# Kernel tuning notes

Measured on AMD Instinct MI355X. Metric: run time of the kernel, lower is better.

## Reference

```python
import jax, jax.numpy as jnp
import numpy as np

SR = 44100
S_TAUS = [10.0, 50.0, 100.0]   # ms
L_TAUS = [500.0, 1500.0, 3000.0]  # ms
EPS = 1e-8


def ms2coef(ms, sr):
    return float(1.0 - np.exp(-2200.0 / (ms * sr)))


def ema(x, coef):
    # First-order leaky integrator y[t] = coef*x[t] + (1-coef)*y[t-1], y[-1]=0.
    # x: [B, T]; scan over time with carry of shape [B].
    coef = jnp.asarray(coef, x.dtype)
    one_m = jnp.asarray(1.0, x.dtype) - coef

    def step(carry, xt):
        y = coef * xt + one_m * carry
        return y, y

    _, ys = jax.lax.scan(step, jnp.zeros(x.shape[0], x.dtype), x.T)
    return ys.T  # [B, T]


def hadamard(x):
    # mid/side transform on channel dim (-2), orthonormal scaling
    m = x[..., 0, :] + x[..., 1, :]
    s = x[..., 0, :] - x[..., 1, :]
    return jnp.stack([m, s], axis=-2) * jnp.asarray(np.sqrt(0.5), x.dtype)


def ldr_feat(x_sq, s_coef, l_coef, shift):
    # log short-term envelope minus (time-aligned) log long-term envelope
    short = jnp.log(ema(x_sq, s_coef))
    long_ = jnp.log(ema(x_sq, l_coef))
    return short - jnp.roll(long_, -shift, axis=-1)


def setup_inputs() -> dict:
    key = jax.random.key(0)
    k1, k2 = jax.random.split(key)
    x_pred = jax.random.normal(k1, (4, 2, 1048576), dtype=jnp.float32)
    x_true = jax.random.normal(k2, (4, 2, 1048576), dtype=jnp.float32)
    return {"x_pred": x_pred, "x_true": x_true}


def reference(x_pred, x_true):
    xp = hadamard(x_pred)
    xt = hadamard(x_true)
    T = xp.shape[-1]
    ps = jnp.clip(jnp.square(xp), EPS, None).reshape(-1, T)
    ts = jnp.clip(jnp.square(xt), EPS, None).reshape(-1, T)
    total = jnp.asarray(0.0, x_pred.dtype)
    for s_ms, l_ms in zip(S_TAUS, L_TAUS):
        sc = ms2coef(s_ms, SR)
        lc = ms2coef(l_ms, SR)
        shift = int(SR * (l_ms - s_ms) * 0.0005)
        fp = ldr_feat(ps, sc, lc, shift)
        ft = ldr_feat(ts, sc, lc, shift)
        total = total + jnp.mean(jnp.abs(fp - ft))
    return total
```

## Files before the change

kernel.cpp:

```cpp
#include <hip/hip_runtime.h>
#include <cmath>


#define T_LEN    1048576
#define CHUNKS   256
#define CLEN     4096
#define NT1      256
#define SEG1     16
#define COLS     65536
#define JMAX     65535
#define EPS_CLIP 1e-8f
#define K2SEG    32
#define K2NSEG   8

struct K1Args {
  float d[6];
  float apw[6][7];
};
struct K2Args {
  float dL[6];
  float dL32[6];
};
struct CarryPack {
  float d[3];
  float apw[3][9];
};

__device__ __constant__ const int D_SHIFT[3] = {10804, 31972, 63945};


__global__ __launch_bounds__(NT1)
void k1_stage(const float* __restrict__ xp, const float* __restrict__ xt,
              float* __restrict__ Eloc, float* __restrict__ Bs,
              float* __restrict__ Bl, int mode, K1Args ka)
{
  int chunk = blockIdx.x, b = blockIdx.y;
  int which = b >> 2, sig = b & 3, tid = threadIdx.x;
  long base = (long)chunk * CLEN + (long)tid * SEG1;
  const float* x0 = (which ? xt : xp) + (long)sig * 2 * T_LEN;
  const float* x1 = x0 + T_LEN;

  float S[12];
#pragma unroll
  for (int j = 0; j < 12; j++) S[j] = 0.f;

#pragma unroll
  for (int i = 0; i < SEG1 / 4; i++) {
    float4 a = *(const float4*)(x0 + base + 4*i);
    float4 c4 = *(const float4*)(x1 + base + 4*i);
    float sm, sp, pm, ps;
#define STEP(CMP) \
    sm = a.CMP + c4.CMP; sp = a.CMP - c4.CMP; \
    pm = fmaxf(0.5f * sm * sm, EPS_CLIP); ps = fmaxf(0.5f * sp * sp, EPS_CLIP); \
    _Pragma("unroll") \
    for (int cf = 0; cf < 6; cf++) { \
      S[cf*2+0] = fmaf(ka.d[cf], S[cf*2+0], pm); \
      S[cf*2+1] = fmaf(ka.d[cf], S[cf*2+1], ps); \
    }
    STEP(x) STEP(y) STEP(z) STEP(w)
#undef STEP
  }

  int lane = tid & 63, w = tid >> 6;
#pragma unroll
  for (int i = 0; i < 6; i++) {
#pragma unroll
    for (int j = 0; j < 12; j++) {
      float up = __shfl_up(S[j], 1u << i, 64);
      if (lane >= (1 << i)) S[j] = fmaf(ka.apw[j >> 1][i], up, S[j]);
    }
  }
  __shared__ float WT[4][12];
  if (lane == 63)
#pragma unroll
    for (int j = 0; j < 12; j++) WT[w][j] = S[j];
  __syncthreads();
  float C[12];
#pragma unroll
  for (int j = 0; j < 12; j++) C[j] = 0.f;
#pragma unroll
  for (int i = 0; i < 4; i++) {
    if (i < w) {
#pragma unroll
      for (int j = 0; j < 12; j++)
        C[j] = fmaf(ka.apw[j >> 1][6], C[j], WT[i][j]);
    }
  }
  float alp[6];
#pragma unroll
  for (int cf = 0; cf < 6; cf++) {
    int e = lane + 1;
    float a = 1.f;
#pragma unroll
    for (int i = 0; i < 7; i++)
      if (e & (1 << i)) a *= ka.apw[cf][i];
    alp[cf] = a;
  }
#pragma unroll
  for (int j = 0; j < 12; j++) S[j] = fmaf(alp[j >> 1], C[j], S[j]);

  long col = (long)chunk * (CLEN / SEG1) + tid;
  long cbase = ((long)sig * COLS + col) * 12 + which * 2;
  if (mode & 2) {
#pragma unroll
    for (int k = 0; k < 3; k++)
      *(float2*)(Bs + cbase + 4*k) = make_float2(S[4*k+0], S[4*k+1]);
  }
  if (mode & 1) {
#pragma unroll
    for (int k = 0; k < 3; k++)
      *(float2*)(Bl + cbase + 4*k) = make_float2(S[4*k+2], S[4*k+3]);
  }
  if (mode != 2 && tid == NT1 - 1) {
#pragma unroll
    for (int cf = 0; cf < 6; cf++)
#pragma unroll
      for (int st = 0; st < 2; st++)
        Eloc[chunk * 96 + (which*8 + sig*2 + st) * 6 + cf] = S[cf*2 + st];
  }
}

__global__ __launch_bounds__(768)
void k2_scan(const float* __restrict__ Eloc, float* __restrict__ Y, K2Args ka)
{
  int col = threadIdx.x;
  int seg = threadIdx.y;
  float dL = ka.dL[col % 6];
  float A  = ka.dL32[col % 6];
  int c0 = seg * K2SEG;

  float yloc[K2SEG];
  float y = 0.f;
#pragma unroll
  for (int i = 0; i < K2SEG; i++) {
    y = fmaf(dL, y, Eloc[(c0 + i) * 96 + col]);
    yloc[i] = y;
  }
  __shared__ float SY[K2NSEG][96];
  SY[seg][col] = y;
  __syncthreads();
  float C = 0.f;
  for (int s = 0; s < seg; s++) C = fmaf(A, C, SY[s][col]);
  float w = dL;
#pragma unroll
  for (int i = 0; i < K2SEG; i++) {
    Y[(c0 + i) * 96 + col] = fmaf(w, C, yloc[i]);
    w *= dL;
  }
}

__global__ __launch_bounds__(256)
void k3_table(const float* __restrict__ Bl, const float* __restrict__ Y,
              float* __restrict__ Etab, CarryPack cp)
{
  int chunk = blockIdx.x, sig = blockIdx.y, tid = threadIdx.x;
  long col = (long)chunk * 256 + tid;

  float Yc[12];
#pragma unroll
  for (int j = 0; j < 12; j++) Yc[j] = 0.f;
  if (chunk > 0) {
    const float* Yp = Y + (chunk - 1) * 96;
    int rm = sig * 2;
#pragma unroll
    for (int k = 0; k < 3; k++) {
      int cf = 2*k + 1;
      Yc[4*k+0] = Yp[rm*6 + cf];       Yc[4*k+1] = Yp[(rm+1)*6 + cf];
      Yc[4*k+2] = Yp[(8+rm)*6 + cf];   Yc[4*k+3] = Yp[(8+rm+1)*6 + cf];
    }
  }
  float fac[3];
#pragma unroll
  for (int k = 0; k < 3; k++) {
    int e = tid + 1;
    float a = 1.f;
#pragma unroll
    for (int i = 0; i < 9; i++)
      if (e & (1 << i)) a *= cp.apw[k][i];
    fac[k] = a;
  }
  long cbase = ((long)sig * COLS + col) * 12;
#pragma unroll
  for (int k = 0; k < 3; k++) {
    float4 bb = *(const float4*)(Bl + cbase + 4*k);
    float y0 = fmaf(fac[k], Yc[4*k+0], bb.x);
    float y1 = fmaf(fac[k], Yc[4*k+1], bb.y);
    float y2 = fmaf(fac[k], Yc[4*k+2], bb.z);
    float y3 = fmaf(fac[k], Yc[4*k+3], bb.w);
    float em = __log2f(y0) - __log2f(y2);
    float es = __log2f(y1) - __log2f(y3);
    long rowm = (long)(k*8 + sig*2);
    Etab[rowm * COLS + col] = em;
    Etab[(rowm+1) * COLS + col] = es;
  }
}

__device__ __forceinline__ float slow_lerp(const float* __restrict__ row, int q)
{
  int qm = q - 15;
  if (qm < 0) return row[0];
  int j = qm >> 4;
  if (j >= JMAX) return row[JMAX];
  float f = (float)(qm & 15) * 0.0625f;
  float a = row[j], b = row[j + 1];
  return fmaf(f, b - a, a);
}

__global__ __launch_bounds__(256)
void k4all(const float* __restrict__ xp, const float* __restrict__ xt,
           const float* __restrict__ Y, const float* __restrict__ Bs,
           const float* __restrict__ Etab, float* __restrict__ part, CarryPack cp)
{
  int chunk = blockIdx.x, sig = blockIdx.y, tid = threadIdx.x;
  long col = (long)chunk * 256 + tid;
  long base = col * 16;

  float Yc[12];
#pragma unroll
  for (int j = 0; j < 12; j++) Yc[j] = 0.f;
  if (chunk > 0) {
    const float* Yp = Y + (chunk - 1) * 96;
    int rm = sig * 2;
#pragma unroll
    for (int k = 0; k < 3; k++) {
      int cf = 2*k;
      Yc[4*k+0] = Yp[rm*6 + cf];       Yc[4*k+1] = Yp[(rm+1)*6 + cf];
      Yc[4*k+2] = Yp[(8+rm)*6 + cf];   Yc[4*k+3] = Yp[(8+rm+1)*6 + cf];
    }
  }
  float y[12];
  if (tid == 0) {
#pragma unroll
    for (int j = 0; j < 12; j++) y[j] = Yc[j];
  } else {
    float fac[3];
#pragma unroll
    for (int k = 0; k < 3; k++) {
      float a = 1.f;
#pragma unroll
      for (int i = 0; i < 8; i++)
        if (tid & (1 << i)) a *= cp.apw[k][i];
      fac[k] = a;
    }
    long pbase = ((long)sig * COLS + (col - 1)) * 12;
#pragma unroll
    for (int k = 0; k < 3; k++) {
      float4 bb = *(const float4*)(Bs + pbase + 4*k);
      y[4*k+0] = fmaf(fac[k], Yc[4*k+0], bb.x);
      y[4*k+1] = fmaf(fac[k], Yc[4*k+1], bb.y);
      y[4*k+2] = fmaf(fac[k], Yc[4*k+2], bb.z);
      y[4*k+3] = fmaf(fac[k], Yc[4*k+3], bb.w);
    }
  }

  float tm0[3], tm1[3], tm2[3], ts0[3], ts1[3], ts2[3];
  int ofs[3], q0a[3]; bool fastp[3];
#pragma unroll
  for (int k = 0; k < 3; k++) {
    int q0 = (int)base + D_SHIFT[k]; if (q0 >= T_LEN) q0 -= T_LEN;
    q0a[k] = q0;
    int qm = q0 - 15;
    bool f = (qm >= 0) && ((qm >> 4) <= JMAX - 2);
    fastp[k] = f;
    const float* Tm = Etab + (long)(k * 8 + sig * 2) * COLS;
    const float* Ts = Tm + COLS;
    int j0 = f ? (qm >> 4) : 0;
    ofs[k] = f ? (qm & 15) : 0;
    tm0[k] = Tm[j0]; tm1[k] = Tm[j0 + 1]; tm2[k] = Tm[j0 + 2];
    ts0[k] = Ts[j0]; ts1[k] = Ts[j0 + 1]; ts2[k] = Ts[j0 + 2];
  }

  const float* p0 = xp + (long)sig * 2 * T_LEN;
  const float* p1 = p0 + T_LEN;
  const float* t0 = xt + (long)sig * 2 * T_LEN;
  const float* t1 = t0 + T_LEN;

  float acc0 = 0.f, acc1 = 0.f;
#pragma unroll
  for (int qt = 0; qt < 4; qt++) {
    float4 a4 = *(const float4*)(p0 + base + 4*qt);
    float4 b4 = *(const float4*)(p1 + base + 4*qt);
    float4 u4 = *(const float4*)(t0 + base + 4*qt);
    float4 w4 = *(const float4*)(t1 + base + 4*qt);
#define SAMP(CI, CMP) { \
      const int m = 4*qt + CI; \
      float sm = a4.CMP + b4.CMP, sd = a4.CMP - b4.CMP; \
      float pm = fmaxf(0.5f*sm*sm, EPS_CLIP), ps = fmaxf(0.5f*sd*sd, EPS_CLIP); \
      float em_ = u4.CMP + w4.CMP, ed_ = u4.CMP - w4.CMP; \
      float qm_ = fmaxf(0.5f*em_*em_, EPS_CLIP), qs_ = fmaxf(0.5f*ed_*ed_, EPS_CLIP); \
      _Pragma("unroll") \
      for (int k = 0; k < 3; k++) { \
        float dd = cp.d[k]; \
        y[4*k+0] = fmaf(dd, y[4*k+0], pm);  y[4*k+1] = fmaf(dd, y[4*k+1], ps); \
        y[4*k+2] = fmaf(dd, y[4*k+2], qm_); y[4*k+3] = fmaf(dd, y[4*k+3], qs_); \
        float Dm = __log2f(y[4*k+0]) - __log2f(y[4*k+2]); \
        float Ds = __log2f(y[4*k+1]) - __log2f(y[4*k+3]); \
        float em, es; \
        if (fastp[k]) { \
          int d0 = ofs[k] + m; \
          bool hi = d0 >= 16; \
          float am = hi ? tm1[k] : tm0[k], bm = hi ? tm2[k] : tm1[k]; \
          float as = hi ? ts1[k] : ts0[k], bs = hi ? ts2[k] : ts1[k]; \
          float f = (float)(d0 - (hi ? 16 : 0)) * 0.0625f; \
          em = fmaf(f, bm - am, am); \
          es = fmaf(f, bs - as, as); \
        } else { \
          int q = q0a[k] + m; if (q >= T_LEN) q -= T_LEN; \
          const float* Tm = Etab + (long)(k * 8 + sig * 2) * COLS; \
          em = slow_lerp(Tm, q); \
          es = slow_lerp(Tm + COLS, q); \
        } \
        acc0 += fabsf(Dm - em); \
        acc1 += fabsf(Ds - es); \
      } \
    }
    SAMP(0,x) SAMP(1,y) SAMP(2,z) SAMP(3,w)
#undef SAMP
  }

  float acc = acc0 + acc1;
#pragma unroll
  for (int off = 32; off > 0; off >>= 1) acc += __shfl_down(acc, off, 64);
  __shared__ float psum[4];
  int lane = tid & 63, w = tid >> 6;
  if (lane == 0) psum[w] = acc;
  __syncthreads();
  if (tid == 0)
    part[sig * CHUNKS + chunk] = psum[0] + psum[1] + psum[2] + psum[3];
}

__global__ void k5_final(const float* __restrict__ part, float* __restrict__ out)
{
  __shared__ double lds[256];
  int tid = threadIdx.x;
  double s = 0.0;
  for (int i = tid; i < 4 * CHUNKS; i += 256) s += (double)part[i];
  lds[tid] = s; __syncthreads();
  for (int o = 128; o > 0; o >>= 1) {
    if (tid < o) lds[tid] += lds[tid + o];
    __syncthreads();
  }
  if (tid == 0)
    out[0] = (float)(lds[0] * (0.6931471805599453 / (8.0 * 1048576.0)));
}

extern "C" void kernel_launch(void* const* d_in, const int* in_sizes, int n_in,
                              void* d_out, int out_size, void* d_ws, size_t ws_size,
                              hipStream_t stream)
{
  (void)in_sizes; (void)n_in; (void)out_size;
  const float* xp = (const float*)d_in[0];
  const float* xt = (const float*)d_in[1];
  float* out = (float*)d_out;
  char* ws = (char*)d_ws;

  const size_t OFF_ELOC = 0;
  const size_t OFF_Y    = 98304;
  const size_t OFF_PART = 196608;
  const size_t OFF_ETAB = 212992;
  const size_t OFF_B    = 6504448;
  const size_t HALF_B   = 4L * COLS * 12 * 4;
  const size_t NEED_FULL = OFF_B + 2 * HALF_B;
  float* Eloc = (float*)(ws + OFF_ELOC);
  float* Ybuf = (float*)(ws + OFF_Y);
  float* part = (float*)(ws + OFF_PART);
  float* Etab = (float*)(ws + OFF_ETAB);
  float* Bsh  = (float*)(ws + OFF_B);
  float* Blo  = (float*)(ws + OFF_B + HALF_B);

  static const double S_MS[3] = {10.0, 50.0, 100.0};
  static const double L_MS[3] = {500.0, 1500.0, 3000.0};

  K1Args k1a; K2Args k2a; CarryPack cpS, cpL;
  for (int k = 0; k < 3; k++) {
    for (int which = 0; which < 2; which++) {
      int idx = 2 * k + which;
      double ms = which ? L_MS[k] : S_MS[k];
      float cF = (float)(1.0 - std::exp(-2200.0 / (ms * 44100.0)));
      float dF = 1.0f - cF;
      k1a.d[idx] = dF;
      double a16 = std::pow((double)dF, 16.0);
      for (int i = 0; i < 7; i++)
        k1a.apw[idx][i] = (float)std::pow(a16, (double)(1 << i));
      k2a.dL[idx]   = (float)std::pow((double)dF, (double)CLEN);
      k2a.dL32[idx] = (float)std::pow((double)dF, (double)CLEN * (double)K2SEG);
      CarryPack& cp = which ? cpL : cpS;
      cp.d[k] = dF;
      for (int i = 0; i < 9; i++)
        cp.apw[k][i] = (float)std::pow(a16, (double)(1 << i));
    }
  }

  bool full = (ws_size >= NEED_FULL);
  if (full) {
    k1_stage<<<dim3(CHUNKS, 8), NT1, 0, stream>>>(xp, xt, Eloc, Bsh, Blo, 3, k1a);
    k2_scan<<<dim3(1), dim3(96, K2NSEG), 0, stream>>>(Eloc, Ybuf, k2a);
    k3_table<<<dim3(CHUNKS, 4), 256, 0, stream>>>(Blo, Ybuf, Etab, cpL);
    k4all<<<dim3(CHUNKS, 4), 256, 0, stream>>>(xp, xt, Ybuf, Bsh, Etab, part, cpS);
  } else {
    k1_stage<<<dim3(CHUNKS, 8), NT1, 0, stream>>>(xp, xt, Eloc, Bsh, Bsh, 1, k1a);
    k2_scan<<<dim3(1), dim3(96, K2NSEG), 0, stream>>>(Eloc, Ybuf, k2a);
    k3_table<<<dim3(CHUNKS, 4), 256, 0, stream>>>(Bsh, Ybuf, Etab, cpL);
    k1_stage<<<dim3(CHUNKS, 8), NT1, 0, stream>>>(xp, xt, Eloc, Bsh, Bsh, 2, k1a);
    k4all<<<dim3(CHUNKS, 4), 256, 0, stream>>>(xp, xt, Ybuf, Bsh, Etab, part, cpS);
  }
  k5_final<<<1, 256, 0, stream>>>(part, out);
}
```

Baseline: 145.2 us.

## Fold carry scan into table kernel and replace final reduce with atomics

Removes the single-block k2_scan launch by having each k3_table block recompute its needed chunk carries serially from Eloc, while one block writes the full Y prefix for k4all. It also drops the k5_final launch by having k4all atomically add scaled partial sums into the output after a memset. This cuts two kernel launches and their serialization gaps. In exchange it adds redundant serial work that grows with chunk index, and float atomics make the summation order nondeterministic.

```diff
diff --git a/kernel.cpp b/kernel.cpp
--- a/kernel.cpp
+++ b/kernel.cpp
@@ -150,8 +150,9 @@
 }
 
 __global__ __launch_bounds__(256)
-void k3_table(const float* __restrict__ Bl, const float* __restrict__ Y,
-              float* __restrict__ Etab, CarryPack cp)
+void k3_table(const float* __restrict__ Bl, const float* __restrict__ Eloc,
+              const float* __restrict__ Y_in, float* __restrict__ Y_out,
+              float* __restrict__ Etab, CarryPack cp, K2Args k2a, int selfY)
 {
   int chunk = blockIdx.x, sig = blockIdx.y, tid = threadIdx.x;
   long col = (long)chunk * 256 + tid;
@@ -159,8 +160,37 @@
   float Yc[12];
 #pragma unroll
   for (int j = 0; j < 12; j++) Yc[j] = 0.f;
-  if (chunk > 0) {
-    const float* Yp = Y + (chunk - 1) * 96;
+
+  if (selfY) {
+    __shared__ float YcS[12];
+    if (chunk > 0) {
+      if (tid < 12) {
+        int k = tid >> 2, q = tid & 3;
+        int row = ((q >> 1) ? 8 : 0) + sig * 2 + (q & 1);
+        int ci = 2 * k + 1;
+        int colE = row * 6 + ci;
+        float dL = k2a.dL[ci];
+        float yv = 0.f;
+#pragma unroll 4
+        for (int c = 0; c < chunk; c++)
+          yv = fmaf(dL, yv, Eloc[c * 96 + colE]);
+        YcS[tid] = yv;
+      }
+      __syncthreads();
+#pragma unroll
+      for (int j = 0; j < 12; j++) Yc[j] = YcS[j];
+    }
+    if (chunk == 0 && sig == 0 && tid < 96) {
+      float dL = k2a.dL[tid % 6];
+      float yv = 0.f;
+#pragma unroll 8
+      for (int c = 0; c < CHUNKS; c++) {
+        yv = fmaf(dL, yv, Eloc[c * 96 + tid]);
+        Y_out[c * 96 + tid] = yv;
+      }
+    }
+  } else if (chunk > 0) {
+    const float* Yp = Y_in + (chunk - 1) * 96;
     int rm = sig * 2;
 #pragma unroll
     for (int k = 0; k < 3; k++) {
@@ -169,6 +199,7 @@
       Yc[4*k+2] = Yp[(8+rm)*6 + cf];   Yc[4*k+3] = Yp[(8+rm+1)*6 + cf];
     }
   }
+
   float fac[3];
 #pragma unroll
   for (int k = 0; k < 3; k++) {
@@ -209,7 +240,8 @@
 __global__ __launch_bounds__(256)
 void k4all(const float* __restrict__ xp, const float* __restrict__ xt,
            const float* __restrict__ Y, const float* __restrict__ Bs,
-           const float* __restrict__ Etab, float* __restrict__ part, CarryPack cp)
+           const float* __restrict__ Etab, float* __restrict__ part, CarryPack cp,
+           float* __restrict__ out, int useAtomic)
 {
   int chunk = blockIdx.x, sig = blockIdx.y, tid = threadIdx.x;
   long col = (long)chunk * 256 + tid;
@@ -325,8 +357,15 @@
   int lane = tid & 63, w = tid >> 6;
   if (lane == 0) psum[w] = acc;
   __syncthreads();
-  if (tid == 0)
-    part[sig * CHUNKS + chunk] = psum[0] + psum[1] + psum[2] + psum[3];
+  if (tid == 0) {
+    float s = psum[0] + psum[1] + psum[2] + psum[3];
+    if (useAtomic) {
+      const float SCALE = (float)(0.6931471805599453 / (8.0 * 1048576.0));
+      atomicAdd(out, s * SCALE);
+    } else {
+      part[sig * CHUNKS + chunk] = s;
+    }
+  }
 }
 
 __global__ void k5_final(const float* __restrict__ part, float* __restrict__ out)
@@ -393,16 +432,20 @@
 
   bool full = (ws_size >= NEED_FULL);
   if (full) {
+    hipMemsetAsync(out, 0, 4, stream);
     k1_stage<<<dim3(CHUNKS, 8), NT1, 0, stream>>>(xp, xt, Eloc, Bsh, Blo, 3, k1a);
-    k2_scan<<<dim3(1), dim3(96, K2NSEG), 0, stream>>>(Eloc, Ybuf, k2a);
-    k3_table<<<dim3(CHUNKS, 4), 256, 0, stream>>>(Blo, Ybuf, Etab, cpL);
-    k4all<<<dim3(CHUNKS, 4), 256, 0, stream>>>(xp, xt, Ybuf, Bsh, Etab, part, cpS);
+    k3_table<<<dim3(CHUNKS, 4), 256, 0, stream>>>(Blo, Eloc, Ybuf, Ybuf, Etab,
+                                                  cpL, k2a, 1);
+    k4all<<<dim3(CHUNKS, 4), 256, 0, stream>>>(xp, xt, Ybuf, Bsh, Etab, part, cpS,
+                                               out, 1);
   } else {
     k1_stage<<<dim3(CHUNKS, 8), NT1, 0, stream>>>(xp, xt, Eloc, Bsh, Bsh, 1, k1a);
     k2_scan<<<dim3(1), dim3(96, K2NSEG), 0, stream>>>(Eloc, Ybuf, k2a);
-    k3_table<<<dim3(CHUNKS, 4), 256, 0, stream>>>(Bsh, Ybuf, Etab, cpL);
+    k3_table<<<dim3(CHUNKS, 4), 256, 0, stream>>>(Bsh, Eloc, Ybuf, Ybuf, Etab,
+                                                  cpL, k2a, 0);
     k1_stage<<<dim3(CHUNKS, 8), NT1, 0, stream>>>(xp, xt, Eloc, Bsh, Bsh, 2, k1a);
-    k4all<<<dim3(CHUNKS, 4), 256, 0, stream>>>(xp, xt, Ybuf, Bsh, Etab, part, cpS);
-  }
-  k5_final<<<1, 256, 0, stream>>>(part, out);
-}
+    k4all<<<dim3(CHUNKS, 4), 256, 0, stream>>>(xp, xt, Ybuf, Bsh, Etab, part, cpS,
+                                               out, 0);
+    k5_final<<<1, 256, 0, stream>>>(part, out);
+  }
+}
```

Result: slower. 172.1 us (+18.5%).
